# Kernel tuning notes

Hardware: AMD Instinct MI355X
Metric: run time of the kernel (lower is better)

## Reference

```python
import jax, jax.numpy as jnp
import numpy as np

L = 512          # profile HMM model length (number of match states)
S = 25           # alphabet size (input_dim)
BATCH = 128
T_LEN = 1024
TINY = np.finfo(np.float32).tiny


def setup_inputs():
    key = jax.random.key(0)
    ks = jax.random.split(key, 18)
    def n(k, shape):
        return 0.1 * jax.random.normal(k, shape, dtype=jnp.float32)
    return {
        "seq": jax.random.randint(ks[0], (BATCH, T_LEN), 0, S),
        "em_kernel": n(ks[1], (L, S)),
        "ins_kernel": n(ks[2], (S,)),
        "flank_kernel": n(ks[3], (1,)),
        "btm": n(ks[4], (L,)),
        "m2e": n(ks[5], (L,)),
        "mtm": n(ks[6], (L - 1,)),
        "m2i": n(ks[7], (L - 1,)),
        "i2m": n(ks[8], (L - 1,)),
        "i2i": n(ks[9], (L - 1,)),
        "mtd": n(ks[10], (L,)),
        "dtm": n(ks[11], (L,)),
        "dtd": n(ks[12], (L - 1,)),
        "lf_loop": n(ks[13], (1,)),
        "lf_exit": n(ks[14], (1,)),
        "e2u": n(ks[15], (1,)),
        "e2r": n(ks[16], (1,)),
        "e2t": n(ks[17], (1,)),
    }


def _build_hmm(em_kernel, ins_kernel, flank_kernel, btm, m2e, mtm, m2i, i2m, i2i,
               mtd, dtm, dtd, lf_loop, lf_exit, e2u, e2r, e2t):
    """Build implicit transition matrix A [q,q], emission matrix B [q,S+1], init dist [q].
    Explicit states begin/end/delete are marginalized out (silent states), yielding the
    implicit transition structure of the profile HMM (match skips via delete chains)."""
    Lm = em_kernel.shape[0]
    q = 2 * Lm + 3                      # LF, M_1..M_L, I_1..I_{L-1}, U, RF, T
    U, RF, TM = 2 * Lm, 2 * Lm + 1, 2 * Lm + 2
    idx = jnp.arange(Lm)
    dt = em_kernel.dtype
    # per-source-state softmax over explicit outgoing edges
    begin_p = jax.nn.softmax(jnp.concatenate([btm, mtd[:1]]))            # begin -> M_j / D_1
    btm_p = begin_p[:Lm]
    mp = jax.nn.softmax(jnp.stack([mtm, m2i, m2e[:Lm - 1], mtd[1:]], axis=-1), axis=-1)
    mtm_p, m2i_p, m2e_p, mtd_mid = mp[:, 0], mp[:, 1], mp[:, 2], mp[:, 3]
    ip = jax.nn.softmax(jnp.stack([i2m, i2i], axis=-1), axis=-1)
    i2m_p, i2i_p = ip[:, 0], ip[:, 1]
    dp = jax.nn.softmax(jnp.stack([dtm[:Lm - 1], dtd], axis=-1), axis=-1)
    dtm_p = jnp.concatenate([dp[:, 0], jnp.ones((1,), dt)])              # D_L -> end with prob 1
    dtd_p = dp[:, 1]
    fp = jax.nn.softmax(jnp.concatenate([lf_loop, lf_exit]))            # shared flank kernels
    floop, fexit = fp[0], fp[1]
    ep = jax.nn.softmax(jnp.concatenate([e2u, e2r, e2t]))               # end -> U / RF / T
    # marginalize silent delete chain. Sk[i,k]: P(src_i => target via deletes),
    # src_0 = begin, src_i = M_i; target M_{k+2} for k<=L-2, end for k=L-1.
    mtd_p = jnp.concatenate([begin_p[Lm:], mtd_mid])                    # begin->D_1, M_i->D_{i+1}
    cp_log = jnp.concatenate([jnp.zeros((1,), dt), jnp.cumsum(jnp.log(dtd_p))])
    Sk = mtd_p[:, None] * jnp.exp(cp_log[None, :] - cp_log[:, None]) * dtm_p[None, :]
    Sk = jnp.where(idx[None, :] >= idx[:, None], Sk, jnp.zeros((), dt))
    enter = btm_p + jnp.pad(Sk[0, :Lm - 1], (1, 0))                      # begin => M_j
    begin_end = Sk[0, Lm - 1]                                            # begin => end (all deleted)
    m2e_tot = jnp.concatenate([m2e_p + Sk[1:, Lm - 1], jnp.ones((1,), dt)])
    A = jnp.zeros((q, q), dt)
    Mblk = jnp.zeros((Lm, Lm), dt).at[idx[:-1], idx[1:]].set(mtm_p)
    Mblk = Mblk.at[0:Lm - 1, 1:Lm].add(Sk[1:Lm, 0:Lm - 1])               # match skips (j>=i+2)
    A = A.at[1:Lm + 1, 1:Lm + 1].set(Mblk)
    A = A.at[0, 0].set(floop)
    A = A.at[0, 1:Lm + 1].set(fexit * enter)
    A = A.at[0, U].set(fexit * begin_end * ep[0])
    A = A.at[0, RF].set(fexit * begin_end * ep[1])
    A = A.at[0, TM].set(fexit * begin_end * ep[2])
    A = A.at[jnp.arange(1, Lm), jnp.arange(Lm + 1, 2 * Lm)].set(m2i_p)   # M_i -> I_i
    A = A.at[1:Lm + 1, U].set(m2e_tot * ep[0])
    A = A.at[1:Lm + 1, RF].set(m2e_tot * ep[1])
    A = A.at[1:Lm + 1, TM].set(m2e_tot * ep[2])
    A = A.at[jnp.arange(Lm + 1, 2 * Lm), jnp.arange(2, Lm + 1)].set(i2m_p)  # I_i -> M_{i+1}
    A = A.at[jnp.arange(Lm + 1, 2 * Lm), jnp.arange(Lm + 1, 2 * Lm)].set(i2i_p)
    A = A.at[U, 1:Lm + 1].set(fexit * enter)
    A = A.at[U, U].set(floop + fexit * begin_end * ep[0])
    A = A.at[U, RF].set(fexit * begin_end * ep[1])
    A = A.at[U, TM].set(fexit * begin_end * ep[2])
    A = A.at[RF, RF].set(floop)
    A = A.at[RF, TM].set(fexit)
    A = A.at[TM, TM].set(1.0)
    # emission matrix per make_default_emission_matrix: [ins; em; ins x (L+1)] rows,
    # softmax, zero pad column, terminal one-hot row -> [2L+3, S+1]
    rows = jnp.concatenate([ins_kernel[None], em_kernel,
                            jnp.tile(ins_kernel[None], (Lm + 1, 1))], axis=0)
    Bm = jax.nn.softmax(rows, axis=-1)
    Bm = jnp.concatenate([Bm, jnp.zeros((2 * Lm + 2, 1), dt)], axis=-1)
    s_alph = em_kernel.shape[1]
    Bm = jnp.concatenate([Bm, jax.nn.one_hot(jnp.array([s_alph]), s_alph + 1, dtype=dt)], axis=0)
    # initial distribution: start in left flank w.p. sigmoid(flank_init), else enter model
    p0 = jax.nn.sigmoid(flank_kernel[0])
    init = jnp.zeros((q,), dt).at[0].set(p0)
    init = init.at[1:Lm + 1].set((1 - p0) * enter)
    init = init.at[U].set((1 - p0) * begin_end * ep[0])
    init = init.at[RF].set((1 - p0) * begin_end * ep[1])
    init = init.at[TM].set((1 - p0) * begin_end * ep[2])
    return A, Bm, init


def _forward(seq, *params):
    A, Bm, init = _build_hmm(*params)
    # emission probs per timestep: matvec(B, one_hot(x)) == column gather
    E = Bm.T[seq]                        # [batch, T, q]
    alpha = init[None, :] * E[:, 0]
    s = alpha.sum(-1, keepdims=True) + TINY
    ll = jnp.log(s[:, 0])
    alpha = alpha / s

    def step(carry, Et):
        a, l = carry
        a = Et * (a @ A)                 # forward-algorithm recurrence + scaling
        sn = a.sum(-1, keepdims=True) + TINY
        return (a / sn, l + jnp.log(sn[:, 0])), None

    (alpha, ll), _ = jax.lax.scan(step, (alpha, ll), jnp.swapaxes(E[:, 1:], 0, 1))
    return ll                            # [batch] sequence log-likelihoods


def reference(seq, em_kernel, ins_kernel, flank_kernel, btm, m2e, mtm, m2i, i2m, i2i,
              mtd, dtm, dtd, lf_loop, lf_exit, e2u, e2r, e2t):
    return _forward(seq, em_kernel, ins_kernel, flank_kernel, btm, m2e, mtm, m2i, i2m,
                    i2i, mtd, dtm, dtd, lf_loop, lf_exit, e2u, e2r, e2t)
```

## Files before the change

kernel.cpp:

```cpp
#include <hip/hip_runtime.h>
#include <math.h>

#define LM 512
#define TLEN 1024
#define TINY_F 1.17549435e-38f

typedef float v2f __attribute__((ext_vector_type(2)));

__device__ __forceinline__ v2f pfma(v2f a, v2f b, v2f c) {
    return __builtin_elementwise_fma(a, b, c);
}
__device__ __forceinline__ v2f vs(float c) { return (v2f){c, c}; }

template<int Ctrl, int RowMask>
__device__ __forceinline__ float fdpp(float oldv, float src) {
    int r = __builtin_amdgcn_update_dpp(
        __builtin_bit_cast(int, oldv), __builtin_bit_cast(int, src),
        Ctrl, RowMask, 0xF, false);
    return __builtin_bit_cast(float, r);
}

template<int Ctrl, int RowMask>
__device__ __forceinline__ float fdppb(float src) {
    int r = __builtin_amdgcn_update_dpp(
        0, __builtin_bit_cast(int, src),
        Ctrl, RowMask, 0xF, true);
    return __builtin_bit_cast(float, r);
}

__device__ __forceinline__ float rdlane63(float v) {
    return __builtin_bit_cast(float,
        __builtin_amdgcn_readlane(__builtin_bit_cast(int, v), 63));
}

__device__ __forceinline__ float wave_sum_to63(float v) {
    v += fdpp<0x111, 0xF>(0.f, v);
    v += fdpp<0x112, 0xF>(0.f, v);
    v += fdpp<0x114, 0xF>(0.f, v);
    v += fdpp<0x118, 0xF>(0.f, v);
    v += fdpp<0x142, 0xA>(0.f, v);
    v += fdpp<0x143, 0xC>(0.f, v);
    return v;
}

__global__ __launch_bounds__(64, 1) void hmm_fused(
    const int* __restrict__ seq,
    const float* __restrict__ em, const float* __restrict__ ins,
    const float* __restrict__ flank, const float* __restrict__ btm,
    const float* __restrict__ m2e, const float* __restrict__ mtm,
    const float* __restrict__ m2i, const float* __restrict__ i2m,
    const float* __restrict__ i2i, const float* __restrict__ mtd,
    const float* __restrict__ dtm, const float* __restrict__ dtd,
    const float* __restrict__ lfl, const float* __restrict__ lfe,
    const float* __restrict__ e2u, const float* __restrict__ e2r,
    const float* __restrict__ e2t,
    float* __restrict__ out)
{
    __shared__ __align__(16) float sEmb[25 * 512];
    __shared__ float sLogEi[32];
    __shared__ __align__(16) int sSeq[TLEN + 4];

    const int lane = threadIdx.x;
    const int b = blockIdx.x;
    const int base = lane * 8;

    {
        const int4* s4 = (const int4*)(seq + b * TLEN);
        int4* d4 = (int4*)sSeq;
#pragma unroll
        for (int k = lane; k < 256; k += 64) d4[k] = s4[k];
        if (lane < 4) sSeq[TLEN + lane] = 0;
    }

    float insp[25];
    {
        float smI = 0.f;
#pragma unroll
        for (int s = 0; s < 25; ++s) smI += expf(ins[s]);
#pragma unroll
        for (int s = 0; s < 25; ++s) insp[s] = expf(ins[s]) / smI;
        if (lane < 25) sLogEi[lane] = log2f(insp[lane]);
    }

    const float flv = expf(lfl[0]), fev = expf(lfe[0]);
    const float fsv = flv + fev;
    const float floop = flv / fsv, fexit = fev / fsv;
    const float eu = expf(e2u[0]), er = expf(e2r[0]), et = expf(e2t[0]);
    const float esv = eu + er + et;
    const float ep0 = eu / esv, ep1 = er / esv;
    const float p0 = 1.0f / (1.0f + expf(-flank[0]));
    const float omp0 = 1.0f - p0;

    float mtm_[8], dtm_[8], wC_[8], mC_[8], dtmM_[8];
    float i2iA[8], m2iSA[8], invNXA[8], m2eA[8], enterA[8];
    {
        float lw[8], plocal[8], ebv[8], m2epJ[8], mtdpJ1[8], lwn[8];
#pragma unroll
        for (int e = 0; e < 8; ++e) {
            const int j = base + e;
            const int jm1 = (j >= 1) ? j - 1 : 0;
            const int jc  = (j < 511) ? j : 510;
            {
                float a = expf(mtm[jm1]), bb = expf(m2i[jm1]);
                float c = expf(m2e[jm1]), d = expf(mtd[jm1 + 1]);
                float s4 = a + bb + c + d;
                mtm_[e] = (j >= 1) ? a / s4 : 0.f;
                wC_[e]  = (j >= 1) ? d / s4 : 0.f;
                float da = expf(dtm[jm1]), db = expf(dtd[jm1]);
                float sd = da + db;
                float dtv = da / sd, mcv = db / sd;
                dtm_[e] = (j >= 1) ? dtv : 0.f;
                mC_[e]  = (j >= 1) ? mcv : 0.f;
                lw[e]   = (j >= 1) ? logf(mcv) : 0.f;
            }
            {
                float a = expf(mtm[jc]), bb = expf(m2i[jc]);
                float c = expf(m2e[jc]), d = expf(mtd[jc + 1]);
                float s4 = a + bb + c + d;
                float m2ip = bb / s4;
                m2epJ[e]  = c / s4;
                mtdpJ1[e] = d / s4;
                float ia = expf(i2m[jc]), ib = expf(i2i[jc]);
                float s2 = ia + ib;
                float i2mp = ia / s2;
                i2iA[e] = (j < 511) ? ib / s2 : 0.f;
                float da = expf(dtm[jc]), db = expf(dtd[jc]);
                float sd = da + db;
                lwn[e] = logf(db / sd);
                float i2mN = (j + 1 < 512) ? i2mp : 1.0f;
                m2iSA[e]  = ((j < 511) ? m2ip : 0.f) * i2mN;
                invNXA[e] = 1.0f / i2mN;
            }
            ebv[e] = expf(btm[j]);
            plocal[e] = (e == 0) ? lw[0] : plocal[e - 1] + lw[e];
        }
        float incl = wave_sum_to63(plocal[7]);
        float excl = fdppb<0x138, 0xF>(incl);
        float cpT  = rdlane63(incl);
        float ebl = ebv[0] + ebv[1] + ebv[2] + ebv[3]
                  + ebv[4] + ebv[5] + ebv[6] + ebv[7];
        float e512 = expf(mtd[0]);
        float tot = rdlane63(wave_sum_to63(ebl)) + e512;
        float mtdp0 = e512 / tot;
#pragma unroll
        for (int e = 0; e < 8; ++e) {
            const int j = base + e;
            float beginp = ebv[e] / tot;
            float cpjm1 = (e == 0) ? excl : excl + plocal[e - 1];
            enterA[e] = beginp
                + ((j >= 1) ? mtdp0 * expf(cpjm1) * dtm_[e] : 0.f);
            float cpj = excl + plocal[e];
            m2eA[e] = (j < 511)
                ? (m2epJ[e] + mtdpJ1[e] * expf(cpT - (cpj + lwn[e])))
                : 1.0f;
        }
        float Mp = mC_[0];
        dtmM_[0] = dtm_[0];
#pragma unroll
        for (int e = 1; e < 8; ++e) { dtmM_[e] = dtm_[e] * Mp; Mp *= mC_[e]; }
    }

    {
#pragma unroll
        for (int e = 0; e < 8; ++e) {
            const int j = base + e;
            const float* row = em + j * 25;
            float r[25], ex[25];
#pragma unroll
            for (int s = 0; s < 25; ++s) r[s] = row[s];
            float mx = r[0];
#pragma unroll
            for (int s = 1; s < 25; ++s) mx = fmaxf(mx, r[s]);
            float sme = 0.f;
#pragma unroll
            for (int s = 0; s < 25; ++s) { ex[s] = expf(r[s] - mx); sme += ex[s]; }
            float inv = 1.0f / sme;
            const int pos = ((e >> 2) << 8) | (lane << 2) | (e & 3);
#pragma unroll
            for (int s = 0; s < 25; ++s)
                sEmb[s * 512 + pos] = (ex[s] * inv) / insp[s];
        }
    }
    __syncthreads();

    float llE;
    {
        float le = 0.f;
#pragma unroll
        for (int k = 0; k < 16; ++k) le += sLogEi[sSeq[lane * 16 + k]];
        llE = rdlane63(wave_sum_to63(le));
    }

    v2f enter2[4], enterF2[4], m2iS2[4], i2i2[4], m2e2[4], dtmM2[4], invNX2[4];
#pragma unroll
    for (int p = 0; p < 4; ++p) {
        enter2[p]  = (v2f){enterA[2*p], enterA[2*p+1]};
        enterF2[p] = enter2[p] * vs(fexit);
        m2iS2[p]   = (v2f){m2iSA[2*p], m2iSA[2*p+1]};
        i2i2[p]    = (v2f){i2iA[2*p],  i2iA[2*p+1]};
        m2e2[p]    = (v2f){m2eA[2*p],  m2eA[2*p+1]};
        dtmM2[p]   = (v2f){dtmM_[2*p], dtmM_[2*p+1]};
        invNX2[p]  = (v2f){invNXA[2*p], invNXA[2*p+1]};
    }
    const v2f floop2 = vs(floop);
    const v2f epv2 = (v2f){ep0, ep1};

    v2f am2[4], ci2[4];
#define AM(e) ((e) & 1 ? am2[(e) >> 1].y : am2[(e) >> 1].x)
#define CI(e) ((e) & 1 ? ci2[(e) >> 1].y : ci2[(e) >> 1].x)

    v2f EmA2[4], EmB2[4];
    {
        int s0 = sSeq[0];
        const float4* c4 = (const float4*)(sEmb + (s0 << 9) + (lane << 2));
        float4 xx = c4[0], yy = c4[64];
        EmA2[0] = (v2f){xx.x, xx.y}; EmA2[1] = (v2f){xx.z, xx.w};
        EmA2[2] = (v2f){yy.x, yy.y}; EmA2[3] = (v2f){yy.z, yy.w};
    }
#pragma unroll
    for (int p = 0; p < 4; ++p) {
        am2[p] = EmA2[p] * vs(omp0) * enter2[p];
        ci2[p] = (v2f){0.f, 0.f};
    }
    v2f GR = (v2f){p0, 0.f};
    float ll2 = llE;

    int symN = sSeq[1];
    {
        const float4* c4 = (const float4*)(sEmb + (symN << 9) + (lane << 2));
        float4 xx = c4[0], yy = c4[64];
        EmA2[0] = (v2f){xx.x, xx.y}; EmA2[1] = (v2f){xx.z, xx.w};
        EmA2[2] = (v2f){yy.x, yy.y}; EmA2[3] = (v2f){yy.z, yy.w};
    }
    symN = sSeq[2];
    int sidx = 3;

#define STEP(EmC2, EmN2, DO_NORM)                                              \
  {                                                                            \
    {                \
      const float4* c4 = (const float4*)(sEmb + (symN << 9) + (lane << 2));    \
      float4 xx = c4[0], yy = c4[64];                                          \
      EmN2[0] = (v2f){xx.x, xx.y}; EmN2[1] = (v2f){xx.z, xx.w};                \
      EmN2[2] = (v2f){yy.x, yy.y}; EmN2[3] = (v2f){yy.z, yy.w};                \
      symN = sSeq[sidx]; ++sidx;                                               \
    }                                                                          \
    float amL = fdppb<0x138, 0xF>(am2[3].y);                                   \
    float ciL = fdppb<0x138, 0xF>(ci2[3].y);                                   \
                 \
    float Apre[8];                                                             \
    Apre[0] = amL * wC_[0];                                                    \
    _Pragma("unroll")                                                          \
    for (int e = 1; e < 8; ++e)                                                \
      Apre[e] = fmaf(Apre[e - 1], mC_[e], AM(e - 1) * wC_[e]);                 \
         \
    float carry = fdppb<0x138, 0xF>(Apre[7]);                                  \
                \
    v2f dv = am2[0] * m2e2[0];                                                 \
    dv = pfma(am2[1], m2e2[1], dv);                                            \
    dv = pfma(am2[2], m2e2[2], dv);                                            \
    dv = pfma(am2[3], m2e2[3], dv);                                            \
    float dsum = rdlane63(wave_sum_to63(dv.x + dv.y));                         \
              \
    float Gold = GR.x;                                                         \
    GR = pfma(vs(dsum), epv2, GR * floop2);                                    \
       \
    v2f tp[4];                                                                 \
    tp[0].x = fmaf(amL, mtm_[0], ciL);                                         \
    tp[0].y = fmaf(AM(0), mtm_[1], CI(0));                                     \
    tp[1].x = fmaf(AM(1), mtm_[2], CI(1));                                     \
    tp[1].y = fmaf(AM(2), mtm_[3], CI(2));                                     \
    tp[2].x = fmaf(AM(3), mtm_[4], CI(3));                                     \
    tp[2].y = fmaf(AM(4), mtm_[5], CI(4));                                     \
    tp[3].x = fmaf(AM(5), mtm_[6], CI(5));                                     \
    tp[3].y = fmaf(AM(6), mtm_[7], CI(6));                                     \
                       \
    ci2[0] = pfma(am2[0], m2iS2[0], ci2[0] * i2i2[0]);                         \
    ci2[1] = pfma(am2[1], m2iS2[1], ci2[1] * i2i2[1]);                         \
    ci2[2] = pfma(am2[2], m2iS2[2], ci2[2] * i2i2[2]);                         \
    ci2[3] = pfma(am2[3], m2iS2[3], ci2[3] * i2i2[3]);                         \
          \
    v2f Gold2 = vs(Gold), carry2 = vs(carry);                                  \
    tp[0] = pfma(Gold2, enterF2[0], tp[0]);                                    \
    tp[1] = pfma(Gold2, enterF2[1], tp[1]);                                    \
    tp[2] = pfma(Gold2, enterF2[2], tp[2]);                                    \
    tp[3] = pfma(Gold2, enterF2[3], tp[3]);                                    \
    tp[0].y = fmaf(dtm_[1], Apre[0], tp[0].y);                                 \
    tp[1].x = fmaf(dtm_[2], Apre[1], tp[1].x);                                 \
    tp[1].y = fmaf(dtm_[3], Apre[2], tp[1].y);                                 \
    tp[2].x = fmaf(dtm_[4], Apre[3], tp[2].x);                                 \
    tp[2].y = fmaf(dtm_[5], Apre[4], tp[2].y);                                 \
    tp[3].x = fmaf(dtm_[6], Apre[5], tp[3].x);                                 \
    tp[3].y = fmaf(dtm_[7], Apre[6], tp[3].y);                                 \
    tp[0] = pfma(dtmM2[0], carry2, tp[0]);                                     \
    tp[1] = pfma(dtmM2[1], carry2, tp[1]);                                     \
    tp[2] = pfma(dtmM2[2], carry2, tp[2]);                                     \
    tp[3] = pfma(dtmM2[3], carry2, tp[3]);                                     \
    am2[0] = EmC2[0] * tp[0];                                                  \
    am2[1] = EmC2[1] * tp[1];                                                  \
    am2[2] = EmC2[2] * tp[2];                                                  \
    am2[3] = EmC2[3] * tp[3];                                                  \
              \
    if (DO_NORM) {                                                             \
      v2f ns = pfma(ci2[0], invNX2[0], am2[0]);                                \
      ns += pfma(ci2[1], invNX2[1], am2[1]);                                   \
      ns += pfma(ci2[2], invNX2[2], am2[2]);                                   \
      ns += pfma(ci2[3], invNX2[3], am2[3]);                                   \
      float sl = ns.x + ns.y + ((lane == 0) ? (GR.x + GR.y) : 0.f);            \
      float s = rdlane63(wave_sum_to63(sl)) + TINY_F;                          \
      ll2 += __log2f(s);                                                       \
      float inv = 1.0f / s;                                                    \
      v2f inv2 = vs(inv);                                                      \
      am2[0] *= inv2; am2[1] *= inv2; am2[2] *= inv2; am2[3] *= inv2;          \
      ci2[0] *= inv2; ci2[1] *= inv2; ci2[2] *= inv2; ci2[3] *= inv2;          \
      GR *= inv2;                                                              \
    }                                                                          \
  }

#define PAIR(NORM2)                                                            \
    STEP(EmA2, EmB2, 0)                                                        \
    STEP(EmB2, EmA2, NORM2)

    for (int c = 0; c < 63; ++c) {
        int nf = ((c & 3) == 3);
        PAIR(0) PAIR(0) PAIR(0) PAIR(0)
        PAIR(0) PAIR(0) PAIR(0) PAIR(nf)
    }
    for (int p = 0; p < 7; ++p) {
        PAIR(0)
    }
    STEP(EmA2, EmB2, 1)
#undef PAIR
#undef STEP
#undef AM
#undef CI

    if (lane == 0) out[b] = ll2 * 0.69314718055994530942f;
}

extern "C" void kernel_launch(void* const* d_in, const int* in_sizes, int n_in,
                              void* d_out, int out_size, void* d_ws, size_t ws_size,
                              hipStream_t stream) {
    const int*   seq   = (const int*)d_in[0];
    const float* em    = (const float*)d_in[1];
    const float* ins   = (const float*)d_in[2];
    const float* flank = (const float*)d_in[3];
    const float* btm   = (const float*)d_in[4];
    const float* m2e   = (const float*)d_in[5];
    const float* mtm   = (const float*)d_in[6];
    const float* m2i   = (const float*)d_in[7];
    const float* i2m   = (const float*)d_in[8];
    const float* i2i   = (const float*)d_in[9];
    const float* mtd   = (const float*)d_in[10];
    const float* dtm   = (const float*)d_in[11];
    const float* dtd   = (const float*)d_in[12];
    const float* lfl   = (const float*)d_in[13];
    const float* lfe   = (const float*)d_in[14];
    const float* e2u   = (const float*)d_in[15];
    const float* e2r   = (const float*)d_in[16];
    const float* e2t   = (const float*)d_in[17];
    float* out = (float*)d_out;
    (void)d_ws; (void)ws_size;

    hipLaunchKernelGGL(hmm_fused, dim3(128), dim3(64), 0, stream,
        seq, em, ins, flank, btm, m2e, mtm, m2i, i2m, i2i, mtd, dtm, dtd,
        lfl, lfe, e2u, e2r, e2t, out);
}
```

Before: 267.2 us.

## Split HMM parameter preparation into separate prep kernel writing to workspace

Moves the per-block construction of emission tables and transition parameters into a small prep kernel (8 blocks) that writes them to a workspace buffer. The forward kernel then loads the precomputed emission table and parameters from global memory instead of recomputing softmaxes and exps redundantly in each of the 128 blocks. This removes repeated transcendental work per block at the cost of an extra kernel launch and a serial dependency between the two launches.

Measured after the change: 264.3 us. About the same (-1.1%).

```diff
diff --git a/kernel.cpp b/kernel.cpp
--- a/kernel.cpp
+++ b/kernel.cpp
@@ -4,6 +4,19 @@
 #define LM 512
 #define TLEN 1024
 #define TINY_F 1.17549435e-38f
+
+#define OFF_ENTER 0
+#define OFF_MTM   512
+#define OFF_I2M   1024
+#define OFF_DTM   1536
+#define OFF_WC    2048
+#define OFF_MC    2560
+#define OFF_M2I   3072
+#define OFF_I2I   3584
+#define OFF_M2E   4096
+#define OFF_INS   4608
+#define OFF_SC    4640
+#define OFF_EMB   5120
 
 typedef float v2f __attribute__((ext_vector_type(2)));
 
@@ -43,8 +56,7 @@
     return v;
 }
 
-__global__ __launch_bounds__(64, 1) void hmm_fused(
-    const int* __restrict__ seq,
+__global__ __launch_bounds__(64) void hmm_prep(
     const float* __restrict__ em, const float* __restrict__ ins,
     const float* __restrict__ flank, const float* __restrict__ btm,
     const float* __restrict__ m2e, const float* __restrict__ mtm,
@@ -53,33 +65,36 @@
     const float* __restrict__ dtm, const float* __restrict__ dtd,
     const float* __restrict__ lfl, const float* __restrict__ lfe,
     const float* __restrict__ e2u, const float* __restrict__ e2r,
-    const float* __restrict__ e2t,
-    float* __restrict__ out)
+    const float* __restrict__ e2t, float* __restrict__ P)
 {
-    __shared__ __align__(16) float sEmb[25 * 512];
-    __shared__ float sLogEi[32];
-    __shared__ __align__(16) int sSeq[TLEN + 4];
-
     const int lane = threadIdx.x;
-    const int b = blockIdx.x;
+    const int j = blockIdx.x * 64 + lane;
+
+    {
+        float sm = 0.f;
+        for (int s = 0; s < 25; ++s) sm += expf(ins[s]);
+        const float* row = em + j * 25;
+        float mx = row[0];
+        for (int s = 1; s < 25; ++s) mx = fmaxf(mx, row[s]);
+        float sme = 0.f;
+        for (int s = 0; s < 25; ++s) sme += expf(row[s] - mx);
+        float inv = 1.0f / sme;
+        int lanej = j >> 3, e = j & 7;
+        int pos = ((e >> 2) << 8) | (lanej << 2) | (e & 3);
+        for (int s = 0; s < 25; ++s) {
+            float inspS = expf(ins[s]) / sm;
+            P[OFF_EMB + s * 512 + pos] = (expf(row[s] - mx) * inv) / inspS;
+        }
+    }
+
+    if (blockIdx.x != 0) return;
+
     const int base = lane * 8;
 
     {
-        const int4* s4 = (const int4*)(seq + b * TLEN);
-        int4* d4 = (int4*)sSeq;
-#pragma unroll
-        for (int k = lane; k < 256; k += 64) d4[k] = s4[k];
-        if (lane < 4) sSeq[TLEN + lane] = 0;
-    }
-
-    float insp[25];
-    {
         float smI = 0.f;
-#pragma unroll
         for (int s = 0; s < 25; ++s) smI += expf(ins[s]);
-#pragma unroll
-        for (int s = 0; s < 25; ++s) insp[s] = expf(ins[s]) / smI;
-        if (lane < 25) sLogEi[lane] = log2f(insp[lane]);
+        if (lane < 25) P[OFF_INS + lane] = log2f(expf(ins[lane]) / smI);
     }
 
     const float flv = expf(lfl[0]), fev = expf(lfe[0]);
@@ -89,29 +104,37 @@
     const float esv = eu + er + et;
     const float ep0 = eu / esv, ep1 = er / esv;
     const float p0 = 1.0f / (1.0f + expf(-flank[0]));
-    const float omp0 = 1.0f - p0;
-
-    float mtm_[8], dtm_[8], wC_[8], mC_[8], dtmM_[8];
+
+    if (lane == 0) {
+        P[OFF_SC + 0] = floop;
+        P[OFF_SC + 1] = fexit;
+        P[OFF_SC + 2] = p0;
+        P[OFF_SC + 5] = ep0;
+        P[OFF_SC + 6] = ep1;
+        P[OFF_SC + 9] = 1.0f - p0;
+    }
+
+    float mtm_[8], dtm_[8], wC_[8], mC_[8];
     float i2iA[8], m2iSA[8], invNXA[8], m2eA[8], enterA[8];
     {
         float lw[8], plocal[8], ebv[8], m2epJ[8], mtdpJ1[8], lwn[8];
 #pragma unroll
         for (int e = 0; e < 8; ++e) {
-            const int j = base + e;
-            const int jm1 = (j >= 1) ? j - 1 : 0;
-            const int jc  = (j < 511) ? j : 510;
+            const int jj = base + e;
+            const int jm1 = (jj >= 1) ? jj - 1 : 0;
+            const int jc  = (jj < 511) ? jj : 510;
             {
                 float a = expf(mtm[jm1]), bb = expf(m2i[jm1]);
                 float c = expf(m2e[jm1]), d = expf(mtd[jm1 + 1]);
                 float s4 = a + bb + c + d;
-                mtm_[e] = (j >= 1) ? a / s4 : 0.f;
-                wC_[e]  = (j >= 1) ? d / s4 : 0.f;
+                mtm_[e] = (jj >= 1) ? a / s4 : 0.f;
+                wC_[e]  = (jj >= 1) ? d / s4 : 0.f;
                 float da = expf(dtm[jm1]), db = expf(dtd[jm1]);
                 float sd = da + db;
                 float dtv = da / sd, mcv = db / sd;
-                dtm_[e] = (j >= 1) ? dtv : 0.f;
-                mC_[e]  = (j >= 1) ? mcv : 0.f;
-                lw[e]   = (j >= 1) ? logf(mcv) : 0.f;
+                dtm_[e] = (jj >= 1) ? dtv : 0.f;
+                mC_[e]  = (jj >= 1) ? mcv : 0.f;
+                lw[e]   = (jj >= 1) ? logf(mcv) : 0.f;
             }
             {
                 float a = expf(mtm[jc]), bb = expf(m2i[jc]);
@@ -123,15 +146,15 @@
                 float ia = expf(i2m[jc]), ib = expf(i2i[jc]);
                 float s2 = ia + ib;
                 float i2mp = ia / s2;
-                i2iA[e] = (j < 511) ? ib / s2 : 0.f;
+                i2iA[e] = (jj < 511) ? ib / s2 : 0.f;
                 float da = expf(dtm[jc]), db = expf(dtd[jc]);
                 float sd = da + db;
                 lwn[e] = logf(db / sd);
-                float i2mN = (j + 1 < 512) ? i2mp : 1.0f;
-                m2iSA[e]  = ((j < 511) ? m2ip : 0.f) * i2mN;
+                float i2mN = (jj + 1 < 512) ? i2mp : 1.0f;
+                m2iSA[e]  = ((jj < 511) ? m2ip : 0.f) * i2mN;
                 invNXA[e] = 1.0f / i2mN;
             }
-            ebv[e] = expf(btm[j]);
+            ebv[e] = expf(btm[jj]);
             plocal[e] = (e == 0) ? lw[0] : plocal[e - 1] + lw[e];
         }
         float incl = wave_sum_to63(plocal[7]);
@@ -144,66 +167,103 @@
         float mtdp0 = e512 / tot;
 #pragma unroll
         for (int e = 0; e < 8; ++e) {
-            const int j = base + e;
+            const int jj = base + e;
             float beginp = ebv[e] / tot;
             float cpjm1 = (e == 0) ? excl : excl + plocal[e - 1];
             enterA[e] = beginp
-                + ((j >= 1) ? mtdp0 * expf(cpjm1) * dtm_[e] : 0.f);
+                + ((jj >= 1) ? mtdp0 * expf(cpjm1) * dtm_[e] : 0.f);
             float cpj = excl + plocal[e];
-            m2eA[e] = (j < 511)
+            m2eA[e] = (jj < 511)
                 ? (m2epJ[e] + mtdpJ1[e] * expf(cpT - (cpj + lwn[e])))
                 : 1.0f;
         }
+    }
+#pragma unroll
+    for (int e = 0; e < 8; ++e) {
+        const int jj = base + e;
+        P[OFF_ENTER + jj] = enterA[e];
+        P[OFF_MTM + jj]   = mtm_[e];
+        P[OFF_DTM + jj]   = dtm_[e];
+        P[OFF_WC + jj]    = wC_[e];
+        P[OFF_MC + jj]    = mC_[e];
+        P[OFF_M2I + jj]   = m2iSA[e];
+        P[OFF_I2M + jj]   = invNXA[e];
+        P[OFF_I2I + jj]   = i2iA[e];
+        P[OFF_M2E + jj]   = m2eA[e];
+    }
+}
+
+__global__ __launch_bounds__(64, 1) void hmm_forward(
+    const int* __restrict__ seq, const float* __restrict__ P,
+    float* __restrict__ out)
+{
+    __shared__ __align__(16) float sEmb[25 * 512];
+    __shared__ float sLogEi[32];
+    __shared__ __align__(16) int sSeq[TLEN + 4];
+
+    const int lane = threadIdx.x;
+    const int b = blockIdx.x;
+    const int base = lane * 8;
+
+    {
+        const float4* src = (const float4*)(P + OFF_EMB);
+        float4* dst = (float4*)sEmb;
+#pragma unroll 5
+        for (int k = lane; k < 25 * 128; k += 64) dst[k] = src[k];
+        if (lane < 32) sLogEi[lane] = P[OFF_INS + (lane < 25 ? lane : 0)];
+        const int4* s4 = (const int4*)(seq + b * TLEN);
+        int4* d4 = (int4*)sSeq;
+#pragma unroll
+        for (int k = lane; k < 256; k += 64) d4[k] = s4[k];
+        if (lane < 4) sSeq[TLEN + lane] = 0;
+    }
+    __syncthreads();
+
+    float llE;
+    {
+        float le = 0.f;
+#pragma unroll
+        for (int k = 0; k < 16; ++k) le += sLogEi[sSeq[lane * 16 + k]];
+        llE = rdlane63(wave_sum_to63(le));
+    }
+
+    float mtm_[8], dtm_[8], wC_[8], mC_[8];
+    v2f enter2[4], enterF2[4], m2iS2[4], i2i2[4], m2e2[4], dtmM2[4], invNX2[4];
+    {
+        float enter_[8], m2iS_[8], i2i_[8], m2e_[8], dtmM_[8], invNX_[8];
+#pragma unroll
+        for (int e = 0; e < 8; ++e) {
+            enter_[e] = P[OFF_ENTER + base + e];
+            mtm_[e]   = P[OFF_MTM + base + e];
+            dtm_[e]   = P[OFF_DTM + base + e];
+            wC_[e]    = P[OFF_WC + base + e];
+            mC_[e]    = P[OFF_MC + base + e];
+            i2i_[e]   = P[OFF_I2I + base + e];
+            m2e_[e]   = P[OFF_M2E + base + e];
+            m2iS_[e]  = P[OFF_M2I + base + e];
+            invNX_[e] = P[OFF_I2M + base + e];
+        }
         float Mp = mC_[0];
         dtmM_[0] = dtm_[0];
 #pragma unroll
         for (int e = 1; e < 8; ++e) { dtmM_[e] = dtm_[e] * Mp; Mp *= mC_[e]; }
-    }
-
-    {
-#pragma unroll
-        for (int e = 0; e < 8; ++e) {
-            const int j = base + e;
-            const float* row = em + j * 25;
-            float r[25], ex[25];
-#pragma unroll
-            for (int s = 0; s < 25; ++s) r[s] = row[s];
-            float mx = r[0];
-#pragma unroll
-            for (int s = 1; s < 25; ++s) mx = fmaxf(mx, r[s]);
-            float sme = 0.f;
-#pragma unroll
-            for (int s = 0; s < 25; ++s) { ex[s] = expf(r[s] - mx); sme += ex[s]; }
-            float inv = 1.0f / sme;
-            const int pos = ((e >> 2) << 8) | (lane << 2) | (e & 3);
-#pragma unroll
-            for (int s = 0; s < 25; ++s)
-                sEmb[s * 512 + pos] = (ex[s] * inv) / insp[s];
+#pragma unroll
+        for (int p = 0; p < 4; ++p) {
+            enter2[p] = (v2f){enter_[2*p], enter_[2*p+1]};
+            m2iS2[p]  = (v2f){m2iS_[2*p],  m2iS_[2*p+1]};
+            i2i2[p]   = (v2f){i2i_[2*p],   i2i_[2*p+1]};
+            m2e2[p]   = (v2f){m2e_[2*p],   m2e_[2*p+1]};
+            dtmM2[p]  = (v2f){dtmM_[2*p],  dtmM_[2*p+1]};
+            invNX2[p] = (v2f){invNX_[2*p], invNX_[2*p+1]};
         }
     }
-    __syncthreads();
-
-    float llE;
-    {
-        float le = 0.f;
-#pragma unroll
-        for (int k = 0; k < 16; ++k) le += sLogEi[sSeq[lane * 16 + k]];
-        llE = rdlane63(wave_sum_to63(le));
-    }
-
-    v2f enter2[4], enterF2[4], m2iS2[4], i2i2[4], m2e2[4], dtmM2[4], invNX2[4];
-#pragma unroll
-    for (int p = 0; p < 4; ++p) {
-        enter2[p]  = (v2f){enterA[2*p], enterA[2*p+1]};
-        enterF2[p] = enter2[p] * vs(fexit);
-        m2iS2[p]   = (v2f){m2iSA[2*p], m2iSA[2*p+1]};
-        i2i2[p]    = (v2f){i2iA[2*p],  i2iA[2*p+1]};
-        m2e2[p]    = (v2f){m2eA[2*p],  m2eA[2*p+1]};
-        dtmM2[p]   = (v2f){dtmM_[2*p], dtmM_[2*p+1]};
-        invNX2[p]  = (v2f){invNXA[2*p], invNXA[2*p+1]};
-    }
+    const float floop = P[OFF_SC + 0], fexit = P[OFF_SC + 1], p0 = P[OFF_SC + 2];
+    const float ep0 = P[OFF_SC + 5], ep1 = P[OFF_SC + 6];
+    const float omp0 = P[OFF_SC + 9];
     const v2f floop2 = vs(floop);
     const v2f epv2 = (v2f){ep0, ep1};
+#pragma unroll
+    for (int p = 0; p < 4; ++p) enterF2[p] = enter2[p] * vs(fexit);
 
     v2f am2[4], ci2[4];
 #define AM(e) ((e) & 1 ? am2[(e) >> 1].y : am2[(e) >> 1].x)
@@ -358,10 +418,11 @@
     const float* e2u   = (const float*)d_in[15];
     const float* e2r   = (const float*)d_in[16];
     const float* e2t   = (const float*)d_in[17];
+    float* P = (float*)d_ws;
     float* out = (float*)d_out;
-    (void)d_ws; (void)ws_size;
-
-    hipLaunchKernelGGL(hmm_fused, dim3(128), dim3(64), 0, stream,
-        seq, em, ins, flank, btm, m2e, mtm, m2i, i2m, i2i, mtd, dtm, dtd,
-        lfl, lfe, e2u, e2r, e2t, out);
-}
+
+    hipLaunchKernelGGL(hmm_prep, dim3(8), dim3(64), 0, stream,
+        em, ins, flank, btm, m2e, mtm, m2i, i2m, i2i, mtd, dtm, dtd,
+        lfl, lfe, e2u, e2r, e2t, P);
+    hipLaunchKernelGGL(hmm_forward, dim3(128), dim3(64), 0, stream, seq, P, out);
+}
```
